# Kernel optimization log

Measured on AMD Instinct MI355X. Metric: run time of the kernel, lower is better.

Reference implementation:

```python
import jax, jax.numpy as jnp
import numpy as np
import math

# dims
B, T, HFEAT, E = 32, 8, 128, 128
NUM_CLS, NUM_GLOBAL = 4, 2
NSP = NUM_CLS + NUM_GLOBAL            # 6 special tokens
SCALES = (1, 4, 8)
WINDOW = 4
NHEAD = 8
DH = E // NHEAD                        # 16
NLAYERS = 2                            # blocks per scale = ceil(6/3)
NS = len(SCALES)
F = 512                                # dim_feedforward
ROPE_BASE = 100000.0
NEG = -1e9


def setup_inputs() -> dict:
    key = jax.random.key(0)
    ks = jax.random.split(key, 16)
    def rn(k, shape, s=0.02):
        return jax.random.normal(k, shape, jnp.float32) * s
    inp = {
        'embeddings': jax.random.normal(ks[0], (B, T, NSP + HFEAT, E), jnp.float32),
        'cls_tokens': rn(ks[1], (NUM_CLS, E)),
        'global_tokens': rn(ks[2], (NUM_GLOBAL, E)),
        'Wq': rn(ks[3], (NS, NLAYERS, E, E)),
        'bq': jnp.zeros((NS, NLAYERS, E), jnp.float32),
        'Wk': rn(ks[4], (NS, NLAYERS, E, E)),
        'bk': jnp.zeros((NS, NLAYERS, E), jnp.float32),
        'Wv': rn(ks[5], (NS, NLAYERS, E, E)),
        'bv': jnp.zeros((NS, NLAYERS, E), jnp.float32),
        'Wo': rn(ks[6], (NS, NLAYERS, E, E)),
        'bo': jnp.zeros((NS, NLAYERS, E), jnp.float32),
        'ln1_g': jnp.ones((NS, NLAYERS, E), jnp.float32),
        'ln1_b': jnp.zeros((NS, NLAYERS, E), jnp.float32),
        'ln2_g': jnp.ones((NS, NLAYERS, E), jnp.float32),
        'ln2_b': jnp.zeros((NS, NLAYERS, E), jnp.float32),
        'W1': rn(ks[7], (NS, NLAYERS, E, F)),
        'b1': jnp.zeros((NS, NLAYERS, F), jnp.float32),
        'W2': rn(ks[8], (NS, NLAYERS, F, E)),
        'b2': jnp.zeros((NS, NLAYERS, E), jnp.float32),
        'out_g': jnp.ones((E,), jnp.float32),
        'out_b': jnp.zeros((E,), jnp.float32),
    }
    return inp


def _layernorm(x, g, b, eps=1e-5):
    mu = x.mean(-1, keepdims=True)
    var = ((x - mu) ** 2).mean(-1, keepdims=True)
    return (x - mu) * jax.lax.rsqrt(var + eps) * g + b


def _rope(x):
    # x: (BT, L, H, DH); rotate-half RoPE over head dim
    L = x.shape[1]
    half = DH // 2
    inv = ROPE_BASE ** (-jnp.arange(half, dtype=jnp.float32) / half)
    ang = jnp.arange(L, dtype=jnp.float32)[:, None] * inv[None, :]   # (L, half)
    cos = jnp.cos(ang)[None, :, None, :]
    sin = jnp.sin(ang)[None, :, None, :]
    x1, x2 = x[..., :half], x[..., half:]
    return jnp.concatenate([x1 * cos - x2 * sin, x1 * sin + x2 * cos], axis=-1)


def _sparse_bias(L):
    # global(first NSP) rows/cols fully connected, others window +-WINDOW, diag allowed
    i = jnp.arange(L)
    allowed = (jnp.abs(i[:, None] - i[None, :]) <= WINDOW) | (i[:, None] < NSP) | (i[None, :] < NSP)
    return jnp.where(allowed, 0.0, NEG).astype(jnp.float32)  # (L, L) additive


def _encoder(x, s, Wq, bq, Wk, bk, Wv, bv, Wo, bo, ln1_g, ln1_b, ln2_g, ln2_b, W1, b1, W2, b2, bias):
    # x: (BT, L, E); pre-norm transformer encoder with RoPE attention
    BT, L, _ = x.shape
    for l in range(NLAYERS):
        h = _layernorm(x, ln1_g[s, l], ln1_b[s, l])
        q = (h @ Wq[s, l] + bq[s, l]).reshape(BT, L, NHEAD, DH)
        k = (h @ Wk[s, l] + bk[s, l]).reshape(BT, L, NHEAD, DH)
        v = (h @ Wv[s, l] + bv[s, l]).reshape(BT, L, NHEAD, DH)
        q, k = _rope(q), _rope(k)
        scores = jnp.einsum('blhd,bmhd->bhlm', q, k) / math.sqrt(DH) + bias[None, None]
        attn = jax.nn.softmax(scores, axis=-1)
        o = jnp.einsum('bhlm,bmhd->blhd', attn, v).reshape(BT, L, E)
        x = x + o @ Wo[s, l] + bo[s, l]
        h2 = _layernorm(x, ln2_g[s, l], ln2_b[s, l])
        x = x + jax.nn.gelu(h2 @ W1[s, l] + b1[s, l]) @ W2[s, l] + b2[s, l]
    return x


def reference(embeddings, cls_tokens, global_tokens, Wq, bq, Wk, bk, Wv, bv, Wo, bo,
              ln1_g, ln1_b, ln2_g, ln2_b, W1, b1, W2, b2, out_g, out_b):
    Bb, Tt, HC, Ee = embeddings.shape
    feats = embeddings[..., NSP:, :]                                 # (B,T,H,E)
    specials = jnp.broadcast_to(
        jnp.concatenate([cls_tokens, global_tokens], axis=0)[None, None],
        (Bb, Tt, NSP, Ee))
    cls_per_scale = []
    for s, g in enumerate(SCALES):
        H = feats.shape[2]
        K = H // g  # H divisible by all scales
        grouped = feats.reshape(Bb, Tt, K, g, Ee).mean(axis=3)       # contiguous mean grouping
        seq = jnp.concatenate([specials, grouped], axis=2)           # (B,T,L,E)
        L = NSP + K
        x = seq.reshape(Bb * Tt, L, Ee)
        bias = _sparse_bias(L)
        out = _encoder(x, s, Wq, bq, Wk, bk, Wv, bv, Wo, bo,
                       ln1_g, ln1_b, ln2_g, ln2_b, W1, b1, W2, b2, bias)
        cls_per_scale.append(out.reshape(Bb, Tt, L, Ee)[..., :NUM_CLS, :])
    cls_out = jnp.stack(cls_per_scale, axis=0).mean(axis=0)          # (B,T,num_cls,E)
    cls_out = _layernorm(cls_out, out_g, out_b)
    return cls_out.reshape(Bb, Tt, NUM_CLS * Ee)
```

## Files before the change

kernel.cpp:

```cpp
#include <hip/hip_runtime.h>
#include <hip/hip_bf16.h>

#define BT     256
#define EDIM   128
#define NSP    6
#define RT     49664
#define O1     34304
#define O2     44032
#define KSTR   20

typedef unsigned short u16;
typedef short s16x8 __attribute__((ext_vector_type(8)));
typedef float f32x4 __attribute__((ext_vector_type(4)));

__device__ __forceinline__ float u2f(u16 u){ union{unsigned i; float f;} v; v.i=((unsigned)u)<<16; return v.f; }
__device__ __forceinline__ u16 f2u(float f){
  union{float f; unsigned i;} v; v.f = f;
  unsigned r = v.i + 0x7FFF + ((v.i >> 16) & 1);
  return (u16)(r >> 16);
}
__device__ __forceinline__ float ldin(const void* p, size_t idx, int flag){
  return flag ? u2f(((const u16*)p)[idx]) : ((const float*)p)[idx];
}
__device__ __forceinline__ void unp8(uint4 v, float* f){
  f[0]=u2f((u16)(v.x)); f[1]=u2f((u16)(v.x>>16));
  f[2]=u2f((u16)(v.y)); f[3]=u2f((u16)(v.y>>16));
  f[4]=u2f((u16)(v.z)); f[5]=u2f((u16)(v.z>>16));
  f[6]=u2f((u16)(v.w)); f[7]=u2f((u16)(v.w>>16));
}

__device__ __forceinline__ void rowinfo(int row, int& s, int& r, int& L, int& g){
  if (row < O1){ s=0; r=row;    L=134; g=1; }
  else if (row < O2){ s=1; r=row-O1; L=38; g=4; }
  else { s=2; r=row-O2; L=22; g=8; }
}

__device__ __forceinline__ float ropeInv(int d){
  const float t[8] = {1.f, 0.23713737f, 0.056234132f, 0.013335214f,
                      3.1622777e-3f, 7.4989421e-4f, 1.7782794e-4f, 4.2169650e-5f};
  return t[d];
}

__device__ __forceinline__ float gelu_f(float x){
  float u = x*(1.5957691216f + 0.0713548162f*x*x);
  return x * __builtin_amdgcn_rcpf(1.f + __expf(-u));
}

__device__ __forceinline__ int dflag(const void* ln1g){
  return (*(const unsigned*)ln1g == 0x3F803F80u) ? 1 : 0;
}

struct CArg { const void* src; unsigned dstoff; unsigned n; unsigned inblk; unsigned outblk; };
struct PrepArgs {
  const void* ln1g;
  CArg c[12];
  const void* ws[4][3];
  unsigned wdst[4];
  int wK[4], wN[4], wNsrc[4];
  u16* stage;
};
__global__ __launch_bounds__(256) void prep_k(PrepArgs pa){
  const int flag = dflag(pa.ln1g);
  const int tid = threadIdx.x;
  if (blockIdx.y == 0){
    for (int i = 0; i < 12; i++){
      const CArg& cc = pa.c[i];
      for (unsigned idx = blockIdx.x*256u + tid; idx < cc.n; idx += 64u*256u){
        unsigned blk = idx / cc.inblk, r = idx % cc.inblk;
        pa.stage[cc.dstoff + blk*cc.outblk + r] =
          flag ? ((const u16*)cc.src)[idx] : f2u(((const float*)cc.src)[idx]);
      }
    }
  } else {
    const int v = blockIdx.y - 1;
    const int K = pa.wK[v], N = pa.wN[v], Nsrc = pa.wNsrc[v];
    u16* dst = pa.stage + pa.wdst[v];
    const int total = 6*K*N;
    for (int idx = blockIdx.x*256 + tid; idx < total; idx += 64*256){
      int blk = idx / (K*N);
      int rem = idx % (K*N);
      int j = rem & 7;
      int t = rem >> 3;
      int n = t % N;
      int ck = t / N;
      int k = ck*8 + j;
      int w2 = n / Nsrc;
      int nn = n - w2*Nsrc;
      size_t sidx = (size_t)blk*K*Nsrc + (size_t)k*Nsrc + nn;
      dst[idx] = flag ? ((const u16*)pa.ws[v][w2])[sidx]
                      : f2u(((const float*)pa.ws[v][w2])[sidx]);
    }
  }
}

__global__ __launch_bounds__(256) void build_k(const void* __restrict__ emb,
                                               const void* __restrict__ cls,
                                               const void* __restrict__ glob,
                                               float* __restrict__ x,
                                               u16* __restrict__ H,
                                               const u16* __restrict__ lnG,
                                               const u16* __restrict__ lnB,
                                               const void* __restrict__ flagSrc)
{
  int flag = dflag(flagSrc);
  int row = blockIdx.x*4 + (threadIdx.x >> 6);
  int lane = threadIdx.x & 63;
  int s, r, L, g; rowinfo(row, s, r, L, g);
  int seq = r / L, pos = r % L;
  float v0, v1;
  if (pos < NSP) {
    const void* src = (pos < 4) ? cls : glob;
    int p = (pos < 4) ? pos : pos - 4;
    v0 = ldin(src, p*EDIM + lane, flag);
    v1 = ldin(src, p*EDIM + 64 + lane, flag);
  } else {
    int k = pos - NSP;
    size_t base = ((size_t)seq*134 + NSP + (size_t)k*g)*EDIM + lane;
    float s0 = 0.f, s1 = 0.f;
    for (int j = 0; j < g; j++) {
      s0 += ldin(emb, base + (size_t)j*EDIM, flag);
      s1 += ldin(emb, base + (size_t)j*EDIM + 64, flag);
    }
    float inv = 1.f/(float)g;
    v0 = s0*inv; v1 = s1*inv;
  }
  x[(size_t)row*EDIM + lane]      = v0;
  x[(size_t)row*EDIM + 64 + lane] = v1;
  float sum = v0 + v1, ss = v0*v0 + v1*v1;
  #pragma unroll
  for (int off = 32; off; off >>= 1) { sum += __shfl_xor(sum, off); ss += __shfl_xor(ss, off); }
  float mu = sum * (1.f/128.f);
  float var = ss * (1.f/128.f) - mu*mu;
  float rs = rsqrtf(var + 1e-5f);
  const u16* gp = lnG + s*2*EDIM;
  const u16* bp = lnB + s*2*EDIM;
  H[(size_t)row*EDIM + lane]      = f2u((v0-mu)*rs*u2f(gp[lane])    + u2f(bp[lane]));
  H[(size_t)row*EDIM + 64 + lane] = f2u((v1-mu)*rs*u2f(gp[64+lane]) + u2f(bp[64+lane]));
}

__global__ __launch_bounds__(256) void qkv_k(
    const u16* __restrict__ A,
    const u16* __restrict__ Wt, const u16* __restrict__ Bias,
    u16* __restrict__ C, int layer)
{
  __shared__ u16 Cs[4][16*136];
  const int row0 = blockIdx.x * 64;
  const int n0 = blockIdx.y * 128;
  const int s = row0 < O1 ? 0 : (row0 < O2 ? 1 : 2);
  const int sl = s*2 + layer;
  const u16* Wp = Wt + (size_t)sl*49152;
  const u16* bp = Bias + (size_t)sl*384 + n0;
  const int tid = threadIdx.x;
  const int lane = tid & 63, w = tid >> 6;
  const int g = lane >> 4, l15 = lane & 15;

  s16x8 af[4];
  {
    const u16* arow = A + (size_t)(row0 + w*16 + l15)*128;
    #pragma unroll
    for (int ks = 0; ks < 4; ks++) af[ks] = *(const s16x8*)(arow + (ks*4 + g)*8);
  }
  const u16* wbase = Wp + ((size_t)g*384 + n0 + l15)*8;

  f32x4 acc[8];
  #pragma unroll
  for (int nt = 0; nt < 8; nt++) acc[nt] = (f32x4){0.f,0.f,0.f,0.f};
  #pragma unroll
  for (int ks = 0; ks < 4; ks++) {
    s16x8 bw[8];
    #pragma unroll
    for (int nt = 0; nt < 8; nt++)
      bw[nt] = *(const s16x8*)(wbase + (size_t)ks*12288 + nt*128);
    #pragma unroll
    for (int nt = 0; nt < 8; nt++)
      acc[nt] = __builtin_amdgcn_mfma_f32_16x16x32_bf16(af[ks], bw[nt], acc[nt], 0, 0, 0);
  }

  float bb[8];
  #pragma unroll
  for (int nt = 0; nt < 8; nt++) bb[nt] = u2f(bp[nt*16 + l15]);

  #pragma unroll
  for (int reg = 0; reg < 4; reg++)
    #pragma unroll
    for (int nt = 0; nt < 8; nt++)
      Cs[w][(g*4+reg)*136 + nt*16 + l15] = f2u(acc[nt][reg] + bb[nt]);

  #pragma unroll
  for (int p = 0; p < 4; p++) {
    int r = p*4 + (lane >> 4);
    int off = l15*8;
    uint4 v = *(const uint4*)&Cs[w][r*136 + off];
    *(uint4*)(C + (size_t)(row0 + w*16 + r)*384 + n0 + off) = v;
  }
}

template<int LNFUSE>
__global__ __launch_bounds__(256) __attribute__((amdgpu_waves_per_eu(2,3))) void woffn_k(
    const u16* __restrict__ A,
    const u16* __restrict__ Wot, const u16* __restrict__ Bo,
    const u16* __restrict__ W1t, const u16* __restrict__ B1,
    const u16* __restrict__ W2t, const u16* __restrict__ B2,
    float* __restrict__ X,
    u16* __restrict__ H,
    const u16* __restrict__ ln2G, const u16* __restrict__ ln2B,
    const u16* __restrict__ ln1G, const u16* __restrict__ ln1B,
    int layer)
{
  __shared__ u16 Hs[4][16*136];
  __shared__ u16 Ts[2][4][16*40];
  const int row0 = blockIdx.x * 64;
  const int s = row0 < O1 ? 0 : (row0 < O2 ? 1 : 2);
  const int sl = s*2 + layer;
  const u16* Wop = Wot + (size_t)sl*16384;
  const u16* bop = Bo  + sl*128;
  const u16* W1p = W1t + (size_t)sl*65536;
  const u16* b1p = B1  + sl*512;
  const u16* W2p = W2t + (size_t)sl*65536;
  const u16* b2p = B2  + sl*128;
  const int tid = threadIdx.x;
  const int lane = tid & 63, w = tid >> 6;
  const int g = lane >> 4, l15 = lane & 15;

  s16x8 af[4];
  {
    const u16* arow = A + (size_t)(row0 + w*16 + l15)*128;
    #pragma unroll
    for (int ks = 0; ks < 4; ks++) af[ks] = *(const s16x8*)(arow + (ks*4 + g)*8);
  }
  const u16* wobase = Wop + ((size_t)g*128 + l15)*8;

  f32x4 acc2[8];
  #pragma unroll
  for (int nt = 0; nt < 8; nt++) acc2[nt] = (f32x4){0.f,0.f,0.f,0.f};
  #pragma unroll
  for (int ks = 0; ks < 4; ks++) {
    s16x8 bw[8];
    #pragma unroll
    for (int nt = 0; nt < 8; nt++)
      bw[nt] = *(const s16x8*)(wobase + ((size_t)ks*4096 + nt*128));
    #pragma unroll
    for (int nt = 0; nt < 8; nt++)
      acc2[nt] = __builtin_amdgcn_mfma_f32_16x16x32_bf16(af[ks], bw[nt], acc2[nt], 0, 0, 0);
  }

  {
    float gam[8], bet[8], bo_[8];
    const u16* gp  = ln2G + sl*EDIM;
    const u16* bp2 = ln2B + sl*EDIM;
    #pragma unroll
    for (int nt = 0; nt < 8; nt++) {
      gam[nt] = u2f(gp[nt*16+l15]); bet[nt] = u2f(bp2[nt*16+l15]);
      bo_[nt] = u2f(bop[nt*16+l15]);
    }
    #pragma unroll
    for (int reg = 0; reg < 4; reg++) {
      int row = row0 + w*16 + g*4 + reg;
      float vals[8], ps = 0.f, pss = 0.f;
      #pragma unroll
      for (int nt = 0; nt < 8; nt++) {
        float v = acc2[nt][reg] + bo_[nt] + X[(size_t)row*128 + nt*16 + l15];
        vals[nt] = v; ps += v; pss += v*v;
      }
      #pragma unroll
      for (int off = 1; off < 16; off <<= 1) { ps += __shfl_xor(ps, off); pss += __shfl_xor(pss, off); }
      float mu = ps * (1.f/128.f);
      float var = pss * (1.f/128.f) - mu*mu;
      float rs = rsqrtf(var + 1e-5f);
      #pragma unroll
      for (int nt = 0; nt < 8; nt++) {
        acc2[nt][reg] = vals[nt];
        Hs[w][(g*4+reg)*136 + nt*16 + l15] = f2u((vals[nt]-mu)*rs*gam[nt] + bet[nt]);
      }
    }
  }

  s16x8 hf[4];
  #pragma unroll
  for (int ks = 0; ks < 4; ks++) hf[ks] = *(const s16x8*)&Hs[w][l15*136 + (ks*4+g)*8];

  const u16* w1base = W1p + ((size_t)g*512 + l15)*8;
  const u16* w2base = W2p + ((size_t)g*128 + l15)*8;

  s16x8 bw1[8];
  #pragma unroll
  for (int ks = 0; ks < 4; ks++)
    #pragma unroll
    for (int nt = 0; nt < 2; nt++)
      bw1[ks*2+nt] = *(const s16x8*)(w1base + (size_t)(ks*2048 + nt*16)*8);

  {
    f32x4 acc1[2];
    acc1[0] = (f32x4){0.f,0.f,0.f,0.f};
    acc1[1] = (f32x4){0.f,0.f,0.f,0.f};
    #pragma unroll
    for (int ks = 0; ks < 4; ks++) {
      acc1[0] = __builtin_amdgcn_mfma_f32_16x16x32_bf16(hf[ks], bw1[ks*2+0], acc1[0], 0, 0, 0);
      acc1[1] = __builtin_amdgcn_mfma_f32_16x16x32_bf16(hf[ks], bw1[ks*2+1], acc1[1], 0, 0, 0);
    }
    #pragma unroll
    for (int ks = 0; ks < 4; ks++)
      #pragma unroll
      for (int nt = 0; nt < 2; nt++)
        bw1[ks*2+nt] = *(const s16x8*)(w1base + (size_t)(ks*2048 + 32 + nt*16)*8);
    #pragma unroll
    for (int nt = 0; nt < 2; nt++) {
      float bb1 = u2f(b1p[nt*16 + l15]);
      #pragma unroll
      for (int reg = 0; reg < 4; reg++)
        Ts[0][w][(g*4+reg)*40 + nt*16 + l15] = f2u(gelu_f(acc1[nt][reg] + bb1));
    }
  }

  #pragma unroll
  for (int i = 1; i < 16; i++) {
    const int f0 = i*32, fp = f0 - 32;
    u16* tsC = &Ts[i & 1][w][0];
    const u16* tsP = &Ts[(i & 1) ^ 1][w][0];

    s16x8 bw2a[4];
    #pragma unroll
    for (int nt = 0; nt < 4; nt++)
      bw2a[nt] = *(const s16x8*)(w2base + (size_t)(fp*16 + nt*16)*8);
    s16x8 af2p = *(const s16x8*)(tsP + l15*40 + g*8);

    f32x4 acc1[2];
    acc1[0] = (f32x4){0.f,0.f,0.f,0.f};
    acc1[1] = (f32x4){0.f,0.f,0.f,0.f};
    #pragma unroll
    for (int ks = 0; ks < 4; ks++) {
      acc1[0] = __builtin_amdgcn_mfma_f32_16x16x32_bf16(hf[ks], bw1[ks*2+0], acc1[0], 0, 0, 0);
      acc1[1] = __builtin_amdgcn_mfma_f32_16x16x32_bf16(hf[ks], bw1[ks*2+1], acc1[1], 0, 0, 0);
    }
    {
      const int fn = (f0 + 32) & 511;
      #pragma unroll
      for (int ks = 0; ks < 4; ks++)
        #pragma unroll
        for (int nt = 0; nt < 2; nt++)
          bw1[ks*2+nt] = *(const s16x8*)(w1base + (size_t)(ks*2048 + fn + nt*16)*8);
    }
    s16x8 bw2b[4];
    #pragma unroll
    for (int nt = 0; nt < 4; nt++)
      bw2b[nt] = *(const s16x8*)(w2base + (size_t)(fp*16 + 64 + nt*16)*8);

    #pragma unroll
    for (int nt = 0; nt < 2; nt++) {
      float bb1 = u2f(b1p[f0 + nt*16 + l15]);
      #pragma unroll
      for (int reg = 0; reg < 4; reg++)
        tsC[(g*4+reg)*40 + nt*16 + l15] = f2u(gelu_f(acc1[nt][reg] + bb1));
    }

    #pragma unroll
    for (int nt = 0; nt < 4; nt++)
      acc2[nt] = __builtin_amdgcn_mfma_f32_16x16x32_bf16(af2p, bw2a[nt], acc2[nt], 0, 0, 0);
    #pragma unroll
    for (int nt = 0; nt < 4; nt++)
      acc2[4+nt] = __builtin_amdgcn_mfma_f32_16x16x32_bf16(af2p, bw2b[nt], acc2[4+nt], 0, 0, 0);
  }

  {
    s16x8 af2p = *(const s16x8*)&Ts[1][w][l15*40 + g*8];
    #pragma unroll
    for (int nt = 0; nt < 8; nt++) {
      s16x8 b = *(const s16x8*)(w2base + (size_t)(480*16 + nt*16)*8);
      acc2[nt] = __builtin_amdgcn_mfma_f32_16x16x32_bf16(af2p, b, acc2[nt], 0, 0, 0);
    }
  }

  float bb2[8];
  #pragma unroll
  for (int nt = 0; nt < 8; nt++) bb2[nt] = u2f(b2p[nt*16 + l15]);

  if (LNFUSE) {
    float gam[8], bet[8];
    const u16* gp  = ln1G + (s*2+1)*EDIM;
    const u16* bpn = ln1B + (s*2+1)*EDIM;
    #pragma unroll
    for (int nt = 0; nt < 8; nt++) { gam[nt] = u2f(gp[nt*16+l15]); bet[nt] = u2f(bpn[nt*16+l15]); }
    #pragma unroll
    for (int reg = 0; reg < 4; reg++) {
      int row = row0 + w*16 + g*4 + reg;
      float vals[8], ps = 0.f, pss = 0.f;
      #pragma unroll
      for (int nt = 0; nt < 8; nt++) {
        float v = acc2[nt][reg] + bb2[nt];
        vals[nt] = v; ps += v; pss += v*v;
      }
      #pragma unroll
      for (int off = 1; off < 16; off <<= 1) { ps += __shfl_xor(ps, off); pss += __shfl_xor(pss, off); }
      float mu = ps * (1.f/128.f);
      float var = pss * (1.f/128.f) - mu*mu;
      float rs = rsqrtf(var + 1e-5f);
      #pragma unroll
      for (int nt = 0; nt < 8; nt++) {
        size_t cidx = (size_t)row*128 + nt*16 + l15;
        X[cidx] = vals[nt];
        H[cidx] = f2u((vals[nt]-mu)*rs*gam[nt] + bet[nt]);
      }
    }
  } else {
    #pragma unroll
    for (int reg = 0; reg < 4; reg++) {
      int row = row0 + w*16 + g*4 + reg;
      #pragma unroll
      for (int nt = 0; nt < 8; nt++) {
        size_t cidx = (size_t)row*128 + nt*16 + l15;
        X[cidx] = acc2[nt][reg] + bb2[nt];
      }
    }
  }
}

__global__ __launch_bounds__(128) void attn_k(const u16* __restrict__ qkv, u16* __restrict__ o)
{
  __shared__ float Ks[134*KSTR];
  __shared__ float Vs[134*KSTR];
  int gseq = blockIdx.x, hd = blockIdx.y;
  int L, base;
  if (gseq < 256)      { L = 134; base = gseq*134; }
  else if (gseq < 512) { L = 38;  base = O1 + (gseq-256)*38; }
  else                 { L = 22;  base = O2 + (gseq-512)*22; }
  int tid = threadIdx.x;
  for (int u = tid; u < L*2; u += 128) {
    int kv = u & 1, row = u >> 1;
    const u16* p = qkv + (size_t)(base+row)*384 + 128 + kv*128 + hd*16;
    uint4 w0 = *(const uint4*)p, w1 = *(const uint4*)(p+8);
    float f[16];
    unp8(w0, f); unp8(w1, f+8);
    if (kv == 0) {
      #pragma unroll
      for (int d = 0; d < 8; d++) {
        float ang = (float)row * ropeInv(d);
        float cs = __cosf(ang), sn = __sinf(ang);
        float a = f[d], b = f[d+8];
        f[d]   = a*cs - b*sn;
        f[d+8] = a*sn + b*cs;
      }
    }
    float* dst = (kv ? Vs : Ks) + row*KSTR;
    #pragma unroll
    for (int d = 0; d < 16; d++) dst[d] = f[d];
  }
  __syncthreads();

  for (int it = tid; it < L - NSP; it += 128) {
    int row = NSP + it;
    const u16* qp = qkv + (size_t)(base+row)*384 + hd*16;
    uint4 w0 = *(const uint4*)qp, w1 = *(const uint4*)(qp+8);
    float q[16]; unp8(w0, q); unp8(w1, q+8);
    #pragma unroll
    for (int d = 0; d < 8; d++) {
      float ang = (float)row * ropeInv(d);
      float cs = __cosf(ang), sn = __sinf(ang);
      float a = q[d], b = q[d+8];
      q[d]   = a*cs - b*sn;
      q[d+8] = a*sn + b*cs;
    }
    float m = -1e30f, l = 0.f, oa[16] = {};
    auto step = [&](int j){
      const float4* kr = (const float4*)(Ks + j*KSTR);
      float4 k0 = kr[0], k1 = kr[1], k2 = kr[2], k3 = kr[3];
      float sc = q[0]*k0.x + q[1]*k0.y + q[2]*k0.z + q[3]*k0.w
               + q[4]*k1.x + q[5]*k1.y + q[6]*k1.z + q[7]*k1.w
               + q[8]*k2.x + q[9]*k2.y + q[10]*k2.z + q[11]*k2.w
               + q[12]*k3.x + q[13]*k3.y + q[14]*k3.z + q[15]*k3.w;
      sc *= 0.25f;
      float nm = fmaxf(m, sc);
      float scale = __expf(m - nm);
      float pexp = __expf(sc - nm);
      l = l*scale + pexp;
      const float4* vr = (const float4*)(Vs + j*KSTR);
      float4 v0 = vr[0], v1 = vr[1], v2 = vr[2], v3 = vr[3];
      oa[0]=oa[0]*scale+pexp*v0.x;  oa[1]=oa[1]*scale+pexp*v0.y;
      oa[2]=oa[2]*scale+pexp*v0.z;  oa[3]=oa[3]*scale+pexp*v0.w;
      oa[4]=oa[4]*scale+pexp*v1.x;  oa[5]=oa[5]*scale+pexp*v1.y;
      oa[6]=oa[6]*scale+pexp*v1.z;  oa[7]=oa[7]*scale+pexp*v1.w;
      oa[8]=oa[8]*scale+pexp*v2.x;  oa[9]=oa[9]*scale+pexp*v2.y;
      oa[10]=oa[10]*scale+pexp*v2.z; oa[11]=oa[11]*scale+pexp*v2.w;
      oa[12]=oa[12]*scale+pexp*v3.x; oa[13]=oa[13]*scale+pexp*v3.y;
      oa[14]=oa[14]*scale+pexp*v3.z; oa[15]=oa[15]*scale+pexp*v3.w;
      m = nm;
    };
    #pragma unroll
    for (int j = 0; j < NSP; j++) step(j);
    int jlo = (row-4 > NSP) ? row-4 : NSP;
    int jhi = (row+4 < L-1) ? row+4 : L-1;
    for (int j = jlo; j <= jhi; j++) step(j);
    float invl = 1.f/l;
    u16* op = o + (size_t)(base+row)*EDIM + hd*16;
    #pragma unroll
    for (int d = 0; d < 16; d++) op[d] = f2u(oa[d]*invl);
  }

  if (tid < 96) {
    int row = tid >> 4;
    int u = tid & 15;
    const u16* qp = qkv + (size_t)(base+row)*384 + hd*16;
    uint4 w0 = *(const uint4*)qp, w1 = *(const uint4*)(qp+8);
    float q[16]; unp8(w0, q); unp8(w1, q+8);
    #pragma unroll
    for (int d = 0; d < 8; d++) {
      float ang = (float)row * ropeInv(d);
      float cs = __cosf(ang), sn = __sinf(ang);
      float a = q[d], b = q[d+8];
      q[d]   = a*cs - b*sn;
      q[d+8] = a*sn + b*cs;
    }
    float m = -1e30f, l = 0.f, oa[16] = {};
    for (int j = u; j < L; j += 16) {
      const float4* kr = (const float4*)(Ks + j*KSTR);
      float4 k0 = kr[0], k1 = kr[1], k2 = kr[2], k3 = kr[3];
      float sc = q[0]*k0.x + q[1]*k0.y + q[2]*k0.z + q[3]*k0.w
               + q[4]*k1.x + q[5]*k1.y + q[6]*k1.z + q[7]*k1.w
               + q[8]*k2.x + q[9]*k2.y + q[10]*k2.z + q[11]*k2.w
               + q[12]*k3.x + q[13]*k3.y + q[14]*k3.z + q[15]*k3.w;
      sc *= 0.25f;
      float nm = fmaxf(m, sc);
      float scale = __expf(m - nm);
      float pexp = __expf(sc - nm);
      l = l*scale + pexp;
      const float4* vr = (const float4*)(Vs + j*KSTR);
      float4 v0 = vr[0], v1 = vr[1], v2 = vr[2], v3 = vr[3];
      oa[0]=oa[0]*scale+pexp*v0.x;  oa[1]=oa[1]*scale+pexp*v0.y;
      oa[2]=oa[2]*scale+pexp*v0.z;  oa[3]=oa[3]*scale+pexp*v0.w;
      oa[4]=oa[4]*scale+pexp*v1.x;  oa[5]=oa[5]*scale+pexp*v1.y;
      oa[6]=oa[6]*scale+pexp*v1.z;  oa[7]=oa[7]*scale+pexp*v1.w;
      oa[8]=oa[8]*scale+pexp*v2.x;  oa[9]=oa[9]*scale+pexp*v2.y;
      oa[10]=oa[10]*scale+pexp*v2.z; oa[11]=oa[11]*scale+pexp*v2.w;
      oa[12]=oa[12]*scale+pexp*v3.x; oa[13]=oa[13]*scale+pexp*v3.y;
      oa[14]=oa[14]*scale+pexp*v3.z; oa[15]=oa[15]*scale+pexp*v3.w;
      m = nm;
    }
    #pragma unroll
    for (int off = 1; off < 16; off <<= 1) {
      float m2 = __shfl_xor(m, off);
      float l2 = __shfl_xor(l, off);
      float nm = fmaxf(m, m2);
      float s1 = __expf(m - nm), s2 = __expf(m2 - nm);
      #pragma unroll
      for (int d = 0; d < 16; d++) {
        float o2 = __shfl_xor(oa[d], off);
        oa[d] = oa[d]*s1 + o2*s2;
      }
      l = l*s1 + l2*s2;
      m = nm;
    }
    if (u == 0) {
      float invl = 1.f/l;
      u16* op = o + (size_t)(base+row)*EDIM + hd*16;
      #pragma unroll
      for (int d = 0; d < 16; d++) op[d] = f2u(oa[d]*invl);
    }
  }
}

__global__ __launch_bounds__(256) void final_k(const float* __restrict__ x,
                                               const u16* __restrict__ G,
                                               const u16* __restrict__ Bt,
                                               void* __restrict__ out,
                                               const void* __restrict__ flagSrc)
{
  int flag = dflag(flagSrc);
  int wid = threadIdx.x >> 6, lane = threadIdx.x & 63;
  int idx = blockIdx.x*4 + wid;
  int seq = idx >> 2, c = idx & 3;
  size_t r0 = ((size_t)seq*134 + c)*EDIM;
  size_t r1 = ((size_t)O1 + (size_t)seq*38 + c)*EDIM;
  size_t r2 = ((size_t)O2 + (size_t)seq*22 + c)*EDIM;
  float v0 = (x[r0+lane]    + x[r1+lane]    + x[r2+lane])    * (1.f/3.f);
  float v1 = (x[r0+64+lane] + x[r1+64+lane] + x[r2+64+lane]) * (1.f/3.f);
  float sum = v0 + v1;
  #pragma unroll
  for (int off = 32; off; off >>= 1) sum += __shfl_xor(sum, off);
  float mu = sum * (1.f/128.f);
  float d0 = v0 - mu, d1 = v1 - mu;
  float var = d0*d0 + d1*d1;
  #pragma unroll
  for (int off = 32; off; off >>= 1) var += __shfl_xor(var, off);
  var *= (1.f/128.f);
  float rs = rsqrtf(var + 1e-5f);
  float o0 = d0*rs*u2f(G[lane])    + u2f(Bt[lane]);
  float o1 = d1*rs*u2f(G[64+lane]) + u2f(Bt[64+lane]);
  size_t oi0 = (size_t)seq*512 + c*128 + lane;
  if (flag) { ((u16*)out)[oi0] = f2u(o0); ((u16*)out)[oi0+64] = f2u(o1); }
  else      { ((float*)out)[oi0] = o0;    ((float*)out)[oi0+64] = o1; }
}

#define S_WQKV 0u
#define S_BQKV 294912u
#define S_WO   297216u
#define S_BO   395520u
#define S_W1   396288u
#define S_B1   789504u
#define S_W2   792576u
#define S_B2   1185792u
#define S_L1G  1186560u
#define S_L1B  1187328u
#define S_L2G  1188096u
#define S_L2B  1188864u
#define S_OG   1189632u
#define S_OB   1189760u

extern "C" void kernel_launch(void* const* d_in, const int* in_sizes, int n_in,
                              void* d_out, int out_size, void* d_ws, size_t ws_size,
                              hipStream_t stream) {
  char* wsb = (char*)d_ws;
  u16*   stage = (u16*)(wsb + 64);
  float* x     = (float*)(wsb + (size_t)2379840);
  u16*   h     = (u16*)(wsb + (size_t)27807808);
  u16*   qkv   = (u16*)(wsb + (size_t)40521792);

  PrepArgs pa;
  pa.ln1g = d_in[11];
  pa.stage = stage;
  CArg list[12] = {
    { d_in[4],  S_BQKV,       768, 128, 384 },
    { d_in[6],  S_BQKV+128u,  768, 128, 384 },
    { d_in[8],  S_BQKV+256u,  768, 128, 384 },
    { d_in[10], S_BO,         768, 128, 128 },
    { d_in[16], S_B1,        3072, 512, 512 },
    { d_in[18], S_B2,         768, 128, 128 },
    { d_in[11], S_L1G,        768, 128, 128 },
    { d_in[12], S_L1B,        768, 128, 128 },
    { d_in[13], S_L2G,        768, 128, 128 },
    { d_in[14], S_L2B,        768, 128, 128 },
    { d_in[19], S_OG,         128, 128, 128 },
    { d_in[20], S_OB,         128, 128, 128 },
  };
  for (int i = 0; i < 12; i++) pa.c[i] = list[i];
  pa.ws[0][0]=d_in[3];  pa.ws[0][1]=d_in[5];  pa.ws[0][2]=d_in[7];
  pa.ws[1][0]=d_in[9];  pa.ws[1][1]=d_in[9];  pa.ws[1][2]=d_in[9];
  pa.ws[2][0]=d_in[15]; pa.ws[2][1]=d_in[15]; pa.ws[2][2]=d_in[15];
  pa.ws[3][0]=d_in[17]; pa.ws[3][1]=d_in[17]; pa.ws[3][2]=d_in[17];
  pa.wdst[0]=S_WQKV; pa.wdst[1]=S_WO; pa.wdst[2]=S_W1; pa.wdst[3]=S_W2;
  pa.wK[0]=128; pa.wN[0]=384; pa.wNsrc[0]=128;
  pa.wK[1]=128; pa.wN[1]=128; pa.wNsrc[1]=128;
  pa.wK[2]=128; pa.wN[2]=512; pa.wNsrc[2]=512;
  pa.wK[3]=512; pa.wN[3]=128; pa.wNsrc[3]=128;

  prep_k<<<dim3(64, 5), 256, 0, stream>>>(pa);

  build_k<<<RT/4, 256, 0, stream>>>(d_in[0], d_in[1], d_in[2], x, h,
                                    stage+S_L1G, stage+S_L1B, d_in[11]);

  for (int l = 0; l < 2; l++) {
    qkv_k<<<dim3(RT/64, 3), 256, 0, stream>>>(h, stage+S_WQKV, stage+S_BQKV, qkv, l);
    attn_k<<<dim3(768, 8), 128, 0, stream>>>(qkv, h);
    if (l == 0)
      woffn_k<1><<<RT/64, 256, 0, stream>>>(h, stage+S_WO, stage+S_BO,
                                            stage+S_W1, stage+S_B1, stage+S_W2, stage+S_B2,
                                            x, h, stage+S_L2G, stage+S_L2B,
                                            stage+S_L1G, stage+S_L1B, 0);
    else
      woffn_k<0><<<RT/64, 256, 0, stream>>>(h, stage+S_WO, stage+S_BO,
                                            stage+S_W1, stage+S_B1, stage+S_W2, stage+S_B2,
                                            x, nullptr, stage+S_L2G, stage+S_L2B,
                                            stage+S_L1G, stage+S_L1B, 1);
  }
  final_k<<<BT, 256, 0, stream>>>(x, stage+S_OG, stage+S_OB, d_out, d_in[11]);
}
```

Before: 343.4 us.

## Stage FFN weight chunks into LDS via async global_load_lds double buffering

The fused Wo+FFN kernel now stages W1/W2 32-column chunks into double-buffered shared memory with direct global-to-LDS loads, with all four waves sharing each chunk instead of every wave loading its own weights into registers. It also moves b1 into LDS, aliases the H and T scratch buffers, and drops the waves_per_eu hint. The aim is to cut redundant global weight traffic and register pressure. In exchange it adds two block barriers per iteration, removes the previous software pipelining between GEMM1 and GEMM2, and uses more LDS, which may lower occupancy.

```diff
diff --git a/kernel.cpp b/kernel.cpp
--- a/kernel.cpp
+++ b/kernel.cpp
@@ -48,6 +48,12 @@
 
 __device__ __forceinline__ int dflag(const void* ln1g){
   return (*(const unsigned*)ln1g == 0x3F803F80u) ? 1 : 0;
+}
+
+typedef const unsigned int __attribute__((address_space(1)))* gas1_t;
+typedef unsigned int __attribute__((address_space(3)))* las3_t;
+__device__ __forceinline__ void gload_lds16(const void* g, void* l){
+  __builtin_amdgcn_global_load_lds((gas1_t)g, (las3_t)l, 16, 0, 0);
 }
 
 struct CArg { const void* src; unsigned dstoff; unsigned n; unsigned inblk; unsigned outblk; };
@@ -196,7 +202,7 @@
 }
 
 template<int LNFUSE>
-__global__ __launch_bounds__(256) __attribute__((amdgpu_waves_per_eu(2,3))) void woffn_k(
+__global__ __launch_bounds__(256) void woffn_k(
     const u16* __restrict__ A,
     const u16* __restrict__ Wot, const u16* __restrict__ Bo,
     const u16* __restrict__ W1t, const u16* __restrict__ B1,
@@ -207,8 +213,9 @@
     const u16* __restrict__ ln1G, const u16* __restrict__ ln1B,
     int layer)
 {
-  __shared__ u16 Hs[4][16*136];
-  __shared__ u16 Ts[2][4][16*40];
+  __shared__ u16 HsTs[4*2176];
+  __shared__ u16 wbuf[2][8192];
+  __shared__ u16 b1s[512];
   const int row0 = blockIdx.x * 64;
   const int s = row0 < O1 ? 0 : (row0 < O2 ? 1 : 2);
   const int sl = s*2 + layer;
@@ -222,6 +229,29 @@
   const int lane = tid & 63, w = tid >> 6;
   const int g = lane >> 4, l15 = lane & 15;
 
+  auto stage_chunk = [&](int f0, int cur){
+    u16* wb = wbuf[cur];
+    if (w < 2) {
+      #pragma unroll
+      for (int j = 0; j < 4; j++) {
+        int base = w*2048 + j*512;
+        int kb = (base >> 8) + (lane >> 5);
+        gload_lds16(W1p + (size_t)kb*4096 + (size_t)(f0 + (lane & 31))*8, wb + base);
+      }
+    } else {
+      #pragma unroll
+      for (int j = 0; j < 4; j++) {
+        int base = (w - 2)*2048 + j*512;
+        gload_lds16(W2p + (size_t)(f0 >> 3)*1024 + base + lane*8, wb + 4096 + base);
+      }
+    }
+  };
+
+  b1s[tid]       = b1p[tid];
+  b1s[tid + 256] = b1p[tid + 256];
+
+  stage_chunk(0, 0);
+
   s16x8 af[4];
   {
     const u16* arow = A + (size_t)(row0 + w*16 + l15)*128;
@@ -244,6 +274,7 @@
       acc2[nt] = __builtin_amdgcn_mfma_f32_16x16x32_bf16(af[ks], bw[nt], acc2[nt], 0, 0, 0);
   }
 
+  u16* Hsw = HsTs + w*2176;
   {
     float gam[8], bet[8], bo_[8];
     const u16* gp  = ln2G + sl*EDIM;
@@ -270,103 +301,56 @@
       #pragma unroll
       for (int nt = 0; nt < 8; nt++) {
         acc2[nt][reg] = vals[nt];
-        Hs[w][(g*4+reg)*136 + nt*16 + l15] = f2u((vals[nt]-mu)*rs*gam[nt] + bet[nt]);
+        Hsw[(g*4+reg)*136 + nt*16 + l15] = f2u((vals[nt]-mu)*rs*gam[nt] + bet[nt]);
       }
     }
   }
 
   s16x8 hf[4];
   #pragma unroll
-  for (int ks = 0; ks < 4; ks++) hf[ks] = *(const s16x8*)&Hs[w][l15*136 + (ks*4+g)*8];
-
-  const u16* w1base = W1p + ((size_t)g*512 + l15)*8;
-  const u16* w2base = W2p + ((size_t)g*128 + l15)*8;
-
-  s16x8 bw1[8];
-  #pragma unroll
-  for (int ks = 0; ks < 4; ks++)
-    #pragma unroll
-    for (int nt = 0; nt < 2; nt++)
-      bw1[ks*2+nt] = *(const s16x8*)(w1base + (size_t)(ks*2048 + nt*16)*8);
-
-  {
+  for (int ks = 0; ks < 4; ks++) hf[ks] = *(const s16x8*)&Hsw[l15*136 + (ks*4+g)*8];
+
+  u16* Tsw = HsTs + w*640;
+
+  asm volatile("s_waitcnt lgkmcnt(0)" ::: "memory");
+
+  #pragma unroll
+  for (int i = 0; i < 16; i++) {
+    __builtin_amdgcn_sched_barrier(0);
+    __builtin_amdgcn_s_barrier();
+    if (i < 15) stage_chunk((i + 1)*32, (i + 1) & 1);
+    if (i < 15) { asm volatile("s_waitcnt vmcnt(4)" ::: "memory"); }
+    else        { asm volatile("s_waitcnt vmcnt(0)" ::: "memory"); }
+    __builtin_amdgcn_s_barrier();
+    __builtin_amdgcn_sched_barrier(0);
+
+    const int f0 = i*32;
+    const u16* wb = wbuf[i & 1];
+
     f32x4 acc1[2];
     acc1[0] = (f32x4){0.f,0.f,0.f,0.f};
     acc1[1] = (f32x4){0.f,0.f,0.f,0.f};
     #pragma unroll
     for (int ks = 0; ks < 4; ks++) {
-      acc1[0] = __builtin_amdgcn_mfma_f32_16x16x32_bf16(hf[ks], bw1[ks*2+0], acc1[0], 0, 0, 0);
-      acc1[1] = __builtin_amdgcn_mfma_f32_16x16x32_bf16(hf[ks], bw1[ks*2+1], acc1[1], 0, 0, 0);
-    }
-    #pragma unroll
-    for (int ks = 0; ks < 4; ks++)
-      #pragma unroll
-      for (int nt = 0; nt < 2; nt++)
-        bw1[ks*2+nt] = *(const s16x8*)(w1base + (size_t)(ks*2048 + 32 + nt*16)*8);
+      const int c = ks*4 + g;
+      #pragma unroll
+      for (int nt = 0; nt < 2; nt++) {
+        s16x8 bf = *(const s16x8*)&wb[c*256 + (nt*16 + l15)*8];
+        acc1[nt] = __builtin_amdgcn_mfma_f32_16x16x32_bf16(hf[ks], bf, acc1[nt], 0, 0, 0);
+      }
+    }
     #pragma unroll
     for (int nt = 0; nt < 2; nt++) {
-      float bb1 = u2f(b1p[nt*16 + l15]);
+      float bb1 = u2f(b1s[f0 + nt*16 + l15]);
       #pragma unroll
       for (int reg = 0; reg < 4; reg++)
-        Ts[0][w][(g*4+reg)*40 + nt*16 + l15] = f2u(gelu_f(acc1[nt][reg] + bb1));
-    }
-  }
-
-  #pragma unroll
-  for (int i = 1; i < 16; i++) {
-    const int f0 = i*32, fp = f0 - 32;
-    u16* tsC = &Ts[i & 1][w][0];
-    const u16* tsP = &Ts[(i & 1) ^ 1][w][0];
-
-    s16x8 bw2a[4];
-    #pragma unroll
-    for (int nt = 0; nt < 4; nt++)
-      bw2a[nt] = *(const s16x8*)(w2base + (size_t)(fp*16 + nt*16)*8);
-    s16x8 af2p = *(const s16x8*)(tsP + l15*40 + g*8);
-
-    f32x4 acc1[2];
-    acc1[0] = (f32x4){0.f,0.f,0.f,0.f};
-    acc1[1] = (f32x4){0.f,0.f,0.f,0.f};
-    #pragma unroll
-    for (int ks = 0; ks < 4; ks++) {
-      acc1[0] = __builtin_amdgcn_mfma_f32_16x16x32_bf16(hf[ks], bw1[ks*2+0], acc1[0], 0, 0, 0);
-      acc1[1] = __builtin_amdgcn_mfma_f32_16x16x32_bf16(hf[ks], bw1[ks*2+1], acc1[1], 0, 0, 0);
-    }
-    {
-      const int fn = (f0 + 32) & 511;
-      #pragma unroll
-      for (int ks = 0; ks < 4; ks++)
-        #pragma unroll
-        for (int nt = 0; nt < 2; nt++)
-          bw1[ks*2+nt] = *(const s16x8*)(w1base + (size_t)(ks*2048 + fn + nt*16)*8);
-    }
-    s16x8 bw2b[4];
-    #pragma unroll
-    for (int nt = 0; nt < 4; nt++)
-      bw2b[nt] = *(const s16x8*)(w2base + (size_t)(fp*16 + 64 + nt*16)*8);
-
-    #pragma unroll
-    for (int nt = 0; nt < 2; nt++) {
-      float bb1 = u2f(b1p[f0 + nt*16 + l15]);
-      #pragma unroll
-      for (int reg = 0; reg < 4; reg++)
-        tsC[(g*4+reg)*40 + nt*16 + l15] = f2u(gelu_f(acc1[nt][reg] + bb1));
-    }
-
-    #pragma unroll
-    for (int nt = 0; nt < 4; nt++)
-      acc2[nt] = __builtin_amdgcn_mfma_f32_16x16x32_bf16(af2p, bw2a[nt], acc2[nt], 0, 0, 0);
-    #pragma unroll
-    for (int nt = 0; nt < 4; nt++)
-      acc2[4+nt] = __builtin_amdgcn_mfma_f32_16x16x32_bf16(af2p, bw2b[nt], acc2[4+nt], 0, 0, 0);
-  }
-
-  {
-    s16x8 af2p = *(const s16x8*)&Ts[1][w][l15*40 + g*8];
+        Tsw[(g*4+reg)*40 + nt*16 + l15] = f2u(gelu_f(acc1[nt][reg] + bb1));
+    }
+    s16x8 af2 = *(const s16x8*)&Tsw[l15*40 + g*8];
     #pragma unroll
     for (int nt = 0; nt < 8; nt++) {
-      s16x8 b = *(const s16x8*)(w2base + (size_t)(480*16 + nt*16)*8);
-      acc2[nt] = __builtin_amdgcn_mfma_f32_16x16x32_bf16(af2p, b, acc2[nt], 0, 0, 0);
+      s16x8 bf = *(const s16x8*)&wb[4096 + g*1024 + (nt*16 + l15)*8];
+      acc2[nt] = __builtin_amdgcn_mfma_f32_16x16x32_bf16(af2, bf, acc2[nt], 0, 0, 0);
     }
   }
 
```

Result: no change. 342.6 us (-0.3%).

## Split FFN hidden dimension across two wave groups in woffn kernel

Applied to the files above, without the earlier changes.

Doubles the woffn block to 512 threads, and each 16-row tile is handled by two waves. Each wave computes half of the 512-wide FFN hidden dimension, then the partial W2 accumulators are reduced through shared memory. The first wave group also does the Wo projection and LayerNorm and shares its result via LDS behind a barrier. This shortens the serial FFN loop per wave and adds parallelism, at the cost of extra barriers, a shared-memory reduction, and idle second-group waves during the Wo phase.

```diff
diff --git a/kernel.cpp b/kernel.cpp
--- a/kernel.cpp
+++ b/kernel.cpp
@@ -196,7 +196,7 @@
 }
 
 template<int LNFUSE>
-__global__ __launch_bounds__(256) __attribute__((amdgpu_waves_per_eu(2,3))) void woffn_k(
+__global__ __launch_bounds__(512) void woffn_k(
     const u16* __restrict__ A,
     const u16* __restrict__ Wot, const u16* __restrict__ Bo,
     const u16* __restrict__ W1t, const u16* __restrict__ B1,
@@ -207,8 +207,10 @@
     const u16* __restrict__ ln1G, const u16* __restrict__ ln1B,
     int layer)
 {
-  __shared__ u16 Hs[4][16*136];
-  __shared__ u16 Ts[2][4][16*40];
+  __shared__ union ShmU {
+    struct { u16 Hs[4][2176]; u16 Ts[2][8][640]; } a;
+    f32x4 Pacc[4][512];
+  } shm;
   const int row0 = blockIdx.x * 64;
   const int s = row0 < O1 ? 0 : (row0 < O2 ? 1 : 2);
   const int sl = s*2 + layer;
@@ -220,31 +222,42 @@
   const u16* b2p = B2  + sl*128;
   const int tid = threadIdx.x;
   const int lane = tid & 63, w = tid >> 6;
+  const int tile = w & 3, role = w >> 2;
   const int g = lane >> 4, l15 = lane & 15;
-
-  s16x8 af[4];
-  {
-    const u16* arow = A + (size_t)(row0 + w*16 + l15)*128;
-    #pragma unroll
-    for (int ks = 0; ks < 4; ks++) af[ks] = *(const s16x8*)(arow + (ks*4 + g)*8);
-  }
-  const u16* wobase = Wop + ((size_t)g*128 + l15)*8;
+  const int fbase = role * 256;
+
+  const u16* w1base = W1p + ((size_t)g*512 + l15)*8;
+  const u16* w2base = W2p + ((size_t)g*128 + l15)*8;
 
   f32x4 acc2[8];
   #pragma unroll
   for (int nt = 0; nt < 8; nt++) acc2[nt] = (f32x4){0.f,0.f,0.f,0.f};
-  #pragma unroll
-  for (int ks = 0; ks < 4; ks++) {
-    s16x8 bw[8];
-    #pragma unroll
-    for (int nt = 0; nt < 8; nt++)
-      bw[nt] = *(const s16x8*)(wobase + ((size_t)ks*4096 + nt*128));
-    #pragma unroll
-    for (int nt = 0; nt < 8; nt++)
-      acc2[nt] = __builtin_amdgcn_mfma_f32_16x16x32_bf16(af[ks], bw[nt], acc2[nt], 0, 0, 0);
-  }
-
-  {
+
+  s16x8 bw1[8];
+  #pragma unroll
+  for (int ks = 0; ks < 4; ks++)
+    #pragma unroll
+    for (int nt = 0; nt < 2; nt++)
+      bw1[ks*2+nt] = *(const s16x8*)(w1base + (size_t)(ks*2048 + fbase + nt*16)*8);
+
+  if (role == 0) {
+    s16x8 af[4];
+    {
+      const u16* arow = A + (size_t)(row0 + tile*16 + l15)*128;
+      #pragma unroll
+      for (int ks = 0; ks < 4; ks++) af[ks] = *(const s16x8*)(arow + (ks*4 + g)*8);
+    }
+    const u16* wobase = Wop + ((size_t)g*128 + l15)*8;
+    #pragma unroll
+    for (int ks = 0; ks < 4; ks++) {
+      s16x8 bw[8];
+      #pragma unroll
+      for (int nt = 0; nt < 8; nt++)
+        bw[nt] = *(const s16x8*)(wobase + ((size_t)ks*4096 + nt*128));
+      #pragma unroll
+      for (int nt = 0; nt < 8; nt++)
+        acc2[nt] = __builtin_amdgcn_mfma_f32_16x16x32_bf16(af[ks], bw[nt], acc2[nt], 0, 0, 0);
+    }
     float gam[8], bet[8], bo_[8];
     const u16* gp  = ln2G + sl*EDIM;
     const u16* bp2 = ln2B + sl*EDIM;
@@ -255,7 +268,7 @@
     }
     #pragma unroll
     for (int reg = 0; reg < 4; reg++) {
-      int row = row0 + w*16 + g*4 + reg;
+      int row = row0 + tile*16 + g*4 + reg;
       float vals[8], ps = 0.f, pss = 0.f;
       #pragma unroll
       for (int nt = 0; nt < 8; nt++) {
@@ -270,24 +283,16 @@
       #pragma unroll
       for (int nt = 0; nt < 8; nt++) {
         acc2[nt][reg] = vals[nt];
-        Hs[w][(g*4+reg)*136 + nt*16 + l15] = f2u((vals[nt]-mu)*rs*gam[nt] + bet[nt]);
-      }
-    }
-  }
+        shm.a.Hs[tile][(g*4+reg)*136 + nt*16 + l15] = f2u((vals[nt]-mu)*rs*gam[nt] + bet[nt]);
+      }
+    }
+  }
+
+  __syncthreads();
 
   s16x8 hf[4];
   #pragma unroll
-  for (int ks = 0; ks < 4; ks++) hf[ks] = *(const s16x8*)&Hs[w][l15*136 + (ks*4+g)*8];
-
-  const u16* w1base = W1p + ((size_t)g*512 + l15)*8;
-  const u16* w2base = W2p + ((size_t)g*128 + l15)*8;
-
-  s16x8 bw1[8];
-  #pragma unroll
-  for (int ks = 0; ks < 4; ks++)
-    #pragma unroll
-    for (int nt = 0; nt < 2; nt++)
-      bw1[ks*2+nt] = *(const s16x8*)(w1base + (size_t)(ks*2048 + nt*16)*8);
+  for (int ks = 0; ks < 4; ks++) hf[ks] = *(const s16x8*)&shm.a.Hs[tile][l15*136 + (ks*4+g)*8];
 
   {
     f32x4 acc1[2];
@@ -302,21 +307,21 @@
     for (int ks = 0; ks < 4; ks++)
       #pragma unroll
       for (int nt = 0; nt < 2; nt++)
-        bw1[ks*2+nt] = *(const s16x8*)(w1base + (size_t)(ks*2048 + 32 + nt*16)*8);
+        bw1[ks*2+nt] = *(const s16x8*)(w1base + (size_t)(ks*2048 + fbase + 32 + nt*16)*8);
     #pragma unroll
     for (int nt = 0; nt < 2; nt++) {
-      float bb1 = u2f(b1p[nt*16 + l15]);
+      float bb1 = u2f(b1p[fbase + nt*16 + l15]);
       #pragma unroll
       for (int reg = 0; reg < 4; reg++)
-        Ts[0][w][(g*4+reg)*40 + nt*16 + l15] = f2u(gelu_f(acc1[nt][reg] + bb1));
-    }
-  }
-
-  #pragma unroll
-  for (int i = 1; i < 16; i++) {
-    const int f0 = i*32, fp = f0 - 32;
-    u16* tsC = &Ts[i & 1][w][0];
-    const u16* tsP = &Ts[(i & 1) ^ 1][w][0];
+        shm.a.Ts[0][w][(g*4+reg)*40 + nt*16 + l15] = f2u(gelu_f(acc1[nt][reg] + bb1));
+    }
+  }
+
+  #pragma unroll
+  for (int i = 1; i < 8; i++) {
+    const int f0 = fbase + i*32, fp = f0 - 32;
+    u16* tsC = &shm.a.Ts[i & 1][w][0];
+    const u16* tsP = &shm.a.Ts[(i & 1) ^ 1][w][0];
 
     s16x8 bw2a[4];
     #pragma unroll
@@ -333,7 +338,7 @@
       acc1[1] = __builtin_amdgcn_mfma_f32_16x16x32_bf16(hf[ks], bw1[ks*2+1], acc1[1], 0, 0, 0);
     }
     {
-      const int fn = (f0 + 32) & 511;
+      const int fn = fbase + ((i + 1) & 7)*32;
       #pragma unroll
       for (int ks = 0; ks < 4; ks++)
         #pragma unroll
@@ -362,13 +367,26 @@
   }
 
   {
-    s16x8 af2p = *(const s16x8*)&Ts[1][w][l15*40 + g*8];
+    const int fp = fbase + 224;
+    s16x8 af2p = *(const s16x8*)&shm.a.Ts[1][w][l15*40 + g*8];
     #pragma unroll
     for (int nt = 0; nt < 8; nt++) {
-      s16x8 b = *(const s16x8*)(w2base + (size_t)(480*16 + nt*16)*8);
+      s16x8 b = *(const s16x8*)(w2base + (size_t)(fp*16 + nt*16)*8);
       acc2[nt] = __builtin_amdgcn_mfma_f32_16x16x32_bf16(af2p, b, acc2[nt], 0, 0, 0);
     }
   }
+
+  __syncthreads();
+
+  if (role == 1) {
+    #pragma unroll
+    for (int j = 0; j < 8; j++) shm.Pacc[tile][j*64 + lane] = acc2[j];
+  }
+  __syncthreads();
+  if (role == 1) return;
+
+  #pragma unroll
+  for (int j = 0; j < 8; j++) acc2[j] += shm.Pacc[tile][j*64 + lane];
 
   float bb2[8];
   #pragma unroll
@@ -382,7 +400,7 @@
     for (int nt = 0; nt < 8; nt++) { gam[nt] = u2f(gp[nt*16+l15]); bet[nt] = u2f(bpn[nt*16+l15]); }
     #pragma unroll
     for (int reg = 0; reg < 4; reg++) {
-      int row = row0 + w*16 + g*4 + reg;
+      int row = row0 + tile*16 + g*4 + reg;
       float vals[8], ps = 0.f, pss = 0.f;
       #pragma unroll
       for (int nt = 0; nt < 8; nt++) {
@@ -404,7 +422,7 @@
   } else {
     #pragma unroll
     for (int reg = 0; reg < 4; reg++) {
-      int row = row0 + w*16 + g*4 + reg;
+      int row = row0 + tile*16 + g*4 + reg;
       #pragma unroll
       for (int nt = 0; nt < 8; nt++) {
         size_t cidx = (size_t)row*128 + nt*16 + l15;
@@ -650,12 +668,12 @@
     qkv_k<<<dim3(RT/64, 3), 256, 0, stream>>>(h, stage+S_WQKV, stage+S_BQKV, qkv, l);
     attn_k<<<dim3(768, 8), 128, 0, stream>>>(qkv, h);
     if (l == 0)
-      woffn_k<1><<<RT/64, 256, 0, stream>>>(h, stage+S_WO, stage+S_BO,
+      woffn_k<1><<<RT/64, 512, 0, stream>>>(h, stage+S_WO, stage+S_BO,
                                             stage+S_W1, stage+S_B1, stage+S_W2, stage+S_B2,
                                             x, h, stage+S_L2G, stage+S_L2B,
                                             stage+S_L1G, stage+S_L1B, 0);
     else
-      woffn_k<0><<<RT/64, 256, 0, stream>>>(h, stage+S_WO, stage+S_BO,
+      woffn_k<0><<<RT/64, 512, 0, stream>>>(h, stage+S_WO, stage+S_BO,
                                             stage+S_W1, stage+S_B1, stage+S_W2, stage+S_B2,
                                             x, nullptr, stage+S_L2G, stage+S_L2B,
                                             stage+S_L1G, stage+S_L1B, 1);
```

After: 358.8 us. 4.5% more time.

## Fuse QKV projection into attention kernel per sequence and head

Applied to the files above, without the earlier changes.

Removes the separate QKV GEMM kernel and its qkv buffer. Each attention block now computes its own head's Q, K and V slice with MFMA from the hidden states, applies RoPE in registers via lane shuffles, and stores the results in shared memory. The attention output goes to a separate buffer instead of overwriting h. This drops one launch and the global write and read of the qkv tensor. In exchange, each block re-reads the full 128-wide hidden rows once per head, runs small single-tile MFMAs with only two waves, and uses more shared memory.

```diff
diff --git a/kernel.cpp b/kernel.cpp
--- a/kernel.cpp
+++ b/kernel.cpp
@@ -138,63 +138,6 @@
   H[(size_t)row*EDIM + 64 + lane] = f2u((v1-mu)*rs*u2f(gp[64+lane]) + u2f(bp[64+lane]));
 }
 
-__global__ __launch_bounds__(256) void qkv_k(
-    const u16* __restrict__ A,
-    const u16* __restrict__ Wt, const u16* __restrict__ Bias,
-    u16* __restrict__ C, int layer)
-{
-  __shared__ u16 Cs[4][16*136];
-  const int row0 = blockIdx.x * 64;
-  const int n0 = blockIdx.y * 128;
-  const int s = row0 < O1 ? 0 : (row0 < O2 ? 1 : 2);
-  const int sl = s*2 + layer;
-  const u16* Wp = Wt + (size_t)sl*49152;
-  const u16* bp = Bias + (size_t)sl*384 + n0;
-  const int tid = threadIdx.x;
-  const int lane = tid & 63, w = tid >> 6;
-  const int g = lane >> 4, l15 = lane & 15;
-
-  s16x8 af[4];
-  {
-    const u16* arow = A + (size_t)(row0 + w*16 + l15)*128;
-    #pragma unroll
-    for (int ks = 0; ks < 4; ks++) af[ks] = *(const s16x8*)(arow + (ks*4 + g)*8);
-  }
-  const u16* wbase = Wp + ((size_t)g*384 + n0 + l15)*8;
-
-  f32x4 acc[8];
-  #pragma unroll
-  for (int nt = 0; nt < 8; nt++) acc[nt] = (f32x4){0.f,0.f,0.f,0.f};
-  #pragma unroll
-  for (int ks = 0; ks < 4; ks++) {
-    s16x8 bw[8];
-    #pragma unroll
-    for (int nt = 0; nt < 8; nt++)
-      bw[nt] = *(const s16x8*)(wbase + (size_t)ks*12288 + nt*128);
-    #pragma unroll
-    for (int nt = 0; nt < 8; nt++)
-      acc[nt] = __builtin_amdgcn_mfma_f32_16x16x32_bf16(af[ks], bw[nt], acc[nt], 0, 0, 0);
-  }
-
-  float bb[8];
-  #pragma unroll
-  for (int nt = 0; nt < 8; nt++) bb[nt] = u2f(bp[nt*16 + l15]);
-
-  #pragma unroll
-  for (int reg = 0; reg < 4; reg++)
-    #pragma unroll
-    for (int nt = 0; nt < 8; nt++)
-      Cs[w][(g*4+reg)*136 + nt*16 + l15] = f2u(acc[nt][reg] + bb[nt]);
-
-  #pragma unroll
-  for (int p = 0; p < 4; p++) {
-    int r = p*4 + (lane >> 4);
-    int off = l15*8;
-    uint4 v = *(const uint4*)&Cs[w][r*136 + off];
-    *(uint4*)(C + (size_t)(row0 + w*16 + r)*384 + n0 + off) = v;
-  }
-}
-
 template<int LNFUSE>
 __global__ __launch_bounds__(256) __attribute__((amdgpu_waves_per_eu(2,3))) void woffn_k(
     const u16* __restrict__ A,
@@ -414,50 +357,64 @@
   }
 }
 
-__global__ __launch_bounds__(128) void attn_k(const u16* __restrict__ qkv, u16* __restrict__ o)
+__global__ __launch_bounds__(128) void attn_k(const u16* __restrict__ h,
+                                              const u16* __restrict__ Wt,
+                                              const u16* __restrict__ Bias,
+                                              u16* __restrict__ o, int layer)
 {
+  __shared__ float Qs[134*KSTR];
   __shared__ float Ks[134*KSTR];
   __shared__ float Vs[134*KSTR];
   int gseq = blockIdx.x, hd = blockIdx.y;
-  int L, base;
-  if (gseq < 256)      { L = 134; base = gseq*134; }
-  else if (gseq < 512) { L = 38;  base = O1 + (gseq-256)*38; }
-  else                 { L = 22;  base = O2 + (gseq-512)*22; }
-  int tid = threadIdx.x;
-  for (int u = tid; u < L*2; u += 128) {
-    int kv = u & 1, row = u >> 1;
-    const u16* p = qkv + (size_t)(base+row)*384 + 128 + kv*128 + hd*16;
-    uint4 w0 = *(const uint4*)p, w1 = *(const uint4*)(p+8);
-    float f[16];
-    unp8(w0, f); unp8(w1, f+8);
-    if (kv == 0) {
-      #pragma unroll
-      for (int d = 0; d < 8; d++) {
-        float ang = (float)row * ropeInv(d);
+  int L, base, s;
+  if (gseq < 256)      { s = 0; L = 134; base = gseq*134; }
+  else if (gseq < 512) { s = 1; L = 38;  base = O1 + (gseq-256)*38; }
+  else                 { s = 2; L = 22;  base = O2 + (gseq-512)*22; }
+  const int sl = s*2 + layer;
+  const u16* Wp = Wt + (size_t)sl*49152;
+  const u16* bp = Bias + (size_t)sl*384;
+  const int tid = threadIdx.x;
+  const int lane = tid & 63, w = tid >> 6;
+  const int g = lane >> 4, l15 = lane & 15;
+  const int NT = (L + 15) >> 4;
+
+  for (int task = w; task < NT*3; task += 2) {
+    int t = task / 3, m = task - t*3;
+    int ar = t*16 + l15; if (ar >= L) ar = L - 1;
+    const u16* arow = h + (size_t)(base + ar)*128;
+    const int c0 = m*128 + hd*16 + l15;
+    f32x4 acc = (f32x4){0.f,0.f,0.f,0.f};
+    #pragma unroll
+    for (int ks = 0; ks < 4; ks++) {
+      s16x8 af = *(const s16x8*)(arow + (ks*4 + g)*8);
+      s16x8 bf = *(const s16x8*)(Wp + ((size_t)(ks*4 + g)*384 + c0)*8);
+      acc = __builtin_amdgcn_mfma_f32_16x16x32_bf16(af, bf, acc, 0, 0, 0);
+    }
+    float bb = u2f(bp[c0]);
+    float* dst = (m == 0) ? Qs : ((m == 1) ? Ks : Vs);
+    #pragma unroll
+    for (int reg = 0; reg < 4; reg++) {
+      int row = t*16 + g*4 + reg;
+      float v = acc[reg] + bb;
+      if (m <= 1) {
+        float other = __shfl_xor(v, 8);
+        float ang = (float)row * ropeInv(l15 & 7);
         float cs = __cosf(ang), sn = __sinf(ang);
-        float a = f[d], b = f[d+8];
-        f[d]   = a*cs - b*sn;
-        f[d+8] = a*sn + b*cs;
-      }
-    }
-    float* dst = (kv ? Vs : Ks) + row*KSTR;
-    #pragma unroll
-    for (int d = 0; d < 16; d++) dst[d] = f[d];
+        v = (l15 < 8) ? (v*cs - other*sn) : (other*sn + v*cs);
+      }
+      if (row < L) dst[row*KSTR + l15] = v;
+    }
   }
   __syncthreads();
 
   for (int it = tid; it < L - NSP; it += 128) {
     int row = NSP + it;
-    const u16* qp = qkv + (size_t)(base+row)*384 + hd*16;
-    uint4 w0 = *(const uint4*)qp, w1 = *(const uint4*)(qp+8);
-    float q[16]; unp8(w0, q); unp8(w1, q+8);
-    #pragma unroll
-    for (int d = 0; d < 8; d++) {
-      float ang = (float)row * ropeInv(d);
-      float cs = __cosf(ang), sn = __sinf(ang);
-      float a = q[d], b = q[d+8];
-      q[d]   = a*cs - b*sn;
-      q[d+8] = a*sn + b*cs;
+    float q[16];
+    {
+      const float4* qp = (const float4*)(Qs + row*KSTR);
+      float4 a = qp[0], b = qp[1], c = qp[2], d = qp[3];
+      q[0]=a.x;q[1]=a.y;q[2]=a.z;q[3]=a.w; q[4]=b.x;q[5]=b.y;q[6]=b.z;q[7]=b.w;
+      q[8]=c.x;q[9]=c.y;q[10]=c.z;q[11]=c.w; q[12]=d.x;q[13]=d.y;q[14]=d.z;q[15]=d.w;
     }
     float m = -1e30f, l = 0.f, oa[16] = {};
     auto step = [&](int j){
@@ -498,16 +455,12 @@
   if (tid < 96) {
     int row = tid >> 4;
     int u = tid & 15;
-    const u16* qp = qkv + (size_t)(base+row)*384 + hd*16;
-    uint4 w0 = *(const uint4*)qp, w1 = *(const uint4*)(qp+8);
-    float q[16]; unp8(w0, q); unp8(w1, q+8);
-    #pragma unroll
-    for (int d = 0; d < 8; d++) {
-      float ang = (float)row * ropeInv(d);
-      float cs = __cosf(ang), sn = __sinf(ang);
-      float a = q[d], b = q[d+8];
-      q[d]   = a*cs - b*sn;
-      q[d+8] = a*sn + b*cs;
+    float q[16];
+    {
+      const float4* qp = (const float4*)(Qs + row*KSTR);
+      float4 a = qp[0], b = qp[1], c = qp[2], d = qp[3];
+      q[0]=a.x;q[1]=a.y;q[2]=a.z;q[3]=a.w; q[4]=b.x;q[5]=b.y;q[6]=b.z;q[7]=b.w;
+      q[8]=c.x;q[9]=c.y;q[10]=c.z;q[11]=c.w; q[12]=d.x;q[13]=d.y;q[14]=d.z;q[15]=d.w;
     }
     float m = -1e30f, l = 0.f, oa[16] = {};
     for (int j = u; j < L; j += 16) {
@@ -611,7 +564,7 @@
   u16*   stage = (u16*)(wsb + 64);
   float* x     = (float*)(wsb + (size_t)2379840);
   u16*   h     = (u16*)(wsb + (size_t)27807808);
-  u16*   qkv   = (u16*)(wsb + (size_t)40521792);
+  u16*   ao    = (u16*)(wsb + (size_t)40521792);
 
   PrepArgs pa;
   pa.ln1g = d_in[11];
@@ -647,15 +600,14 @@
                                     stage+S_L1G, stage+S_L1B, d_in[11]);
 
   for (int l = 0; l < 2; l++) {
-    qkv_k<<<dim3(RT/64, 3), 256, 0, stream>>>(h, stage+S_WQKV, stage+S_BQKV, qkv, l);
-    attn_k<<<dim3(768, 8), 128, 0, stream>>>(qkv, h);
+    attn_k<<<dim3(768, 8), 128, 0, stream>>>(h, stage+S_WQKV, stage+S_BQKV, ao, l);
     if (l == 0)
-      woffn_k<1><<<RT/64, 256, 0, stream>>>(h, stage+S_WO, stage+S_BO,
+      woffn_k<1><<<RT/64, 256, 0, stream>>>(ao, stage+S_WO, stage+S_BO,
                                             stage+S_W1, stage+S_B1, stage+S_W2, stage+S_B2,
                                             x, h, stage+S_L2G, stage+S_L2B,
                                             stage+S_L1G, stage+S_L1B, 0);
     else
-      woffn_k<0><<<RT/64, 256, 0, stream>>>(h, stage+S_WO, stage+S_BO,
+      woffn_k<0><<<RT/64, 256, 0, stream>>>(ao, stage+S_WO, stage+S_BO,
                                             stage+S_W1, stage+S_B1, stage+S_W2, stage+S_B2,
                                             x, nullptr, stage+S_L2G, stage+S_L2B,
                                             stage+S_L1G, stage+S_L1B, 1);
```

Result: slower. 415.3 us (+20.9%).
